# Kernel tuning notes

Hardware: AMD Instinct MI355X
Metric: run time of the kernel (lower is better)

## Reference

```python
import jax, jax.numpy as jnp
import numpy as np

K_KP = 4            # sample_keypoints
RADIUS = 2.0        # sample_radius_m
FEATURE_LEVELS = 2
NUM_HEADS = 8


def _keypoints():
    return jnp.array([[0.0, 0.0, 0.0], [RADIUS, 0.0, 0.0],
                      [0.0, RADIUS, 0.0], [-RADIUS, 0.0, 0.0]], jnp.float32)[:K_KP]


def _bilinear(fmap, grid):
    # fmap [C,H,W], grid [N,2] in [-1,1], align_corners=True, zero padding
    C, H, W = fmap.shape
    x = (grid[:, 0] + 1.0) * 0.5 * (W - 1)
    y = (grid[:, 1] + 1.0) * 0.5 * (H - 1)
    x0 = jnp.floor(x); y0 = jnp.floor(y)
    wx1 = x - x0; wx0 = 1.0 - wx1
    wy1 = y - y0; wy0 = 1.0 - wy1

    def get(xi, yi):
        inb = (xi >= 0) & (xi <= W - 1) & (yi >= 0) & (yi <= H - 1)
        xc = jnp.clip(xi, 0, W - 1).astype(jnp.int32)
        yc = jnp.clip(yi, 0, H - 1).astype(jnp.int32)
        return fmap[:, yc, xc] * inb.astype(fmap.dtype)  # [C,N]

    out = (get(x0, y0) * (wx0 * wy0) + get(x0 + 1, y0) * (wx1 * wy0)
           + get(x0, y0 + 1) * (wx0 * wy1) + get(x0 + 1, y0 + 1) * (wx1 * wy1))
    return out.T  # [N,C]


def _sample_level(fmap, refs, intrinsics, extrinsics):
    # fmap [B,V,C,H,W], refs [B,N,3] with N = Q*K_KP
    B, V, C, H, W = fmap.shape
    N = refs.shape[1]
    ph = jnp.concatenate([refs, jnp.ones((B, N, 1), refs.dtype)], -1)     # [B,N,4]
    cam = jnp.einsum('bvij,bnj->bvni', extrinsics, ph)[..., :3]            # [B,V,N,3]
    uvw = jnp.einsum('bvij,bvnj->bvni', intrinsics, cam)                   # [B,V,N,3]
    z = uvw[..., 2]
    zs = jnp.where(jnp.abs(z) > 1e-6, z, 1e-6)
    gx = 2.0 * (uvw[..., 0] / zs) / (W - 1) - 1.0
    gy = 2.0 * (uvw[..., 1] / zs) / (H - 1) - 1.0
    grid = jnp.stack([gx, gy], -1)                                         # [B,V,N,2]
    samp = jax.vmap(jax.vmap(_bilinear))(fmap, grid)                       # [B,V,N,C]
    valid = (z > 0.0).astype(fmap.dtype)                                   # [B,V,N]
    Q = N // K_KP
    samp = samp.reshape(B, V, Q, K_KP, C)
    valid = valid.reshape(B, V, Q, K_KP)
    s = jnp.einsum('bvqkc,bvqk->bqc', samp, valid)
    cnt = jnp.maximum(valid.sum(axis=(1, 3)), 1.0)[..., None]              # [B,Q,1]
    return s / cnt


def _sampler(features, refs_xyz, intrinsics, extrinsics):
    B, Q = refs_xyz.shape[:2]
    refs = (refs_xyz[:, :, None, :] + _keypoints()[None, None]).reshape(B, Q * K_KP, 3)
    out = jnp.zeros((B, Q, features[0].shape[2]), refs_xyz.dtype)
    for fmap in features[:FEATURE_LEVELS]:
        out = out + _sample_level(fmap, refs, intrinsics, extrinsics)
    return out / float(FEATURE_LEVELS)


def _cross_attn(q_in, ctx, Wq, bq, Wk, bk, Wv, bv, Wo, bo):
    B, Qn, D = q_in.shape
    Kn = ctx.shape[1]
    hd = D // NUM_HEADS
    q = (q_in @ Wq.T + bq).reshape(B, Qn, NUM_HEADS, hd).transpose(0, 2, 1, 3)
    k = (ctx @ Wk.T + bk).reshape(B, Kn, NUM_HEADS, hd).transpose(0, 2, 1, 3)
    v = (ctx @ Wv.T + bv).reshape(B, Kn, NUM_HEADS, hd).transpose(0, 2, 1, 3)
    scores = jnp.einsum('bhqd,bhkd->bhqk', q, k) / jnp.sqrt(jnp.asarray(hd, q.dtype))
    attn = jax.nn.softmax(scores, axis=-1)
    o = jnp.einsum('bhqk,bhkd->bhqd', attn, v).transpose(0, 2, 1, 3).reshape(B, Qn, D)
    return o @ Wo.T + bo


def setup_inputs() -> dict:
    key = jax.random.key(0)
    ks = jax.random.split(key, 10)
    B, V, C, Q = 2, 6, 256, 900
    features0 = jax.random.normal(ks[0], (B, V, C, 64, 176), jnp.float32)
    features1 = jax.random.normal(ks[1], (B, V, C, 32, 88), jnp.float32)
    refs_xyz = jax.random.uniform(ks[2], (B, Q, 3), jnp.float32, -1.0, 1.0) * jnp.array([50.0, 50.0, 1.5])
    K = np.array([[1000.0, 0.0, 800.0], [0.0, 1000.0, 450.0], [0.0, 0.0, 1.0]], np.float32)
    intrinsics = jnp.asarray(np.broadcast_to(K, (B, V, 3, 3)).copy())
    axes = np.array([[0.0, -1.0, 0.0], [0.0, 0.0, -1.0], [1.0, 0.0, 0.0]], np.float32)
    exts = np.zeros((V, 4, 4), np.float32)
    for vi in range(V):
        yaw = 2.0 * np.pi * vi / V
        Rz = np.array([[np.cos(yaw), np.sin(yaw), 0.0], [-np.sin(yaw), np.cos(yaw), 0.0], [0.0, 0.0, 1.0]], np.float32)
        exts[vi, :3, :3] = axes @ Rz
        exts[vi, 3, 3] = 1.0
    extrinsics = jnp.asarray(np.broadcast_to(exts, (B, V, 4, 4)).copy())
    queries = jax.random.normal(ks[3], (B, Q, C), jnp.float32)
    Wq = jax.random.normal(ks[4], (C, C), jnp.float32) * 0.02
    Wk = jax.random.normal(ks[5], (C, C), jnp.float32) * 0.02
    Wv = jax.random.normal(ks[6], (C, C), jnp.float32) * 0.02
    Wo = jax.random.normal(ks[7], (C, C), jnp.float32) * 0.02
    z = jnp.zeros((C,), jnp.float32)
    return {"features0": features0, "features1": features1, "refs_xyz": refs_xyz,
            "intrinsics": intrinsics, "extrinsics": extrinsics, "queries": queries,
            "Wq": Wq, "bq": z, "Wk": Wk, "bk": z, "Wv": Wv, "bv": z, "Wo": Wo, "bo": z}


def reference(features0, features1, refs_xyz, intrinsics, extrinsics, queries,
              Wq, bq, Wk, bk, Wv, bv, Wo, bo):
    sampled = _sampler([features0, features1], refs_xyz, intrinsics, extrinsics)  # [B,Q,C]
    return _cross_attn(queries, sampled, Wq, bq, Wk, bk, Wv, bv, Wo, bo)
```

## Files before the change

### kernel.cpp

```cpp
#include <hip/hip_runtime.h>
#include <math.h>

#define B 2
#define V 6
#define C 256
#define Q 900
#define NH 8
#define HD 32
#define RADIUS 2.0f
#define M_ROWS (B * Q)
#define NT 29
#define SPLITS 4
#define TPS 8
#define RBH (B * NH * Q)

using short8 = __attribute__((ext_vector_type(8))) short;
using f32x4  = __attribute__((ext_vector_type(4))) float;

__device__ __forceinline__ short f2bf(float f) {
    union { float f; unsigned u; } x; x.f = f;
    unsigned r = x.u + 0x7fffu + ((x.u >> 16) & 1u);
    return (short)(r >> 16);
}

__device__ __forceinline__ float kpx(int k) { return (k == 1) ? RADIUS : ((k == 3) ? -RADIUS : 0.f); }
__device__ __forceinline__ float kpy(int k) { return (k == 2) ? RADIUS : 0.f; }

__global__ __launch_bounds__(256)
void sampler_kernel(const float* __restrict__ f0, const float* __restrict__ f1,
                    const float* __restrict__ refs, const float* __restrict__ intr,
                    const float* __restrict__ extr, float* __restrict__ sampled)
{
    int b = blockIdx.x / Q, q = blockIdx.x % Q;
    int t = threadIdx.x;
    __shared__ float sx0[2][24], sy0[2][24], swx1[2][24], swy1[2][24];
    __shared__ float sval[24];

    if (t < 48) {
        int lvl = t / 24, pt = t % 24;
        int v = pt >> 2, kp = pt & 3;
        const float* r = refs + (size_t)(b * Q + q) * 3;
        float px = r[0] + kpx(kp), py = r[1] + kpy(kp), pz = r[2];
        const float* E = extr + (size_t)(b * V + v) * 16;
        float cx = E[0] * px + E[1] * py + E[2]  * pz + E[3];
        float cy = E[4] * px + E[5] * py + E[6]  * pz + E[7];
        float cz = E[8] * px + E[9] * py + E[10] * pz + E[11];
        const float* Km = intr + (size_t)(b * V + v) * 9;
        float u = Km[0] * cx + Km[1] * cy + Km[2] * cz;
        float w = Km[3] * cx + Km[4] * cy + Km[5] * cz;
        float z = Km[6] * cx + Km[7] * cy + Km[8] * cz;
        float zs = (fabsf(z) > 1e-6f) ? z : 1e-6f;
        float ru = u / zs, rv = w / zs;
        const float Wf = lvl ? 87.f : 175.f;
        const float Hf = lvl ? 31.f : 63.f;
        float gx = 2.f * ru / Wf - 1.f;
        float gy = 2.f * rv / Hf - 1.f;
        float x = (gx + 1.f) * 0.5f * Wf;
        float y = (gy + 1.f) * 0.5f * Hf;
        float x0 = floorf(x), y0 = floorf(y);
        sx0[lvl][pt] = x0;  sy0[lvl][pt] = y0;
        swx1[lvl][pt] = x - x0;  swy1[lvl][pt] = y - y0;
        if (lvl == 0) sval[pt] = (z > 0.f) ? 1.f : 0.f;
    }
    __syncthreads();

    float cnt = 0.f;
    #pragma unroll
    for (int i = 0; i < 24; ++i) cnt += sval[i];
    cnt = fmaxf(cnt, 1.f);
    float icnt = 1.f / cnt;

    const int xi = t & 1;
    const int cb = t >> 1;
    const float xif = (float)xi;
    float acc0 = 0.f, acc1 = 0.f;

    #pragma unroll
    for (int lvl = 0; lvl < 2; ++lvl) {
        const int H = lvl ? 32 : 64;
        const int W = lvl ? 88 : 176;
        const int HW = H * W;
        const float* fm = lvl ? f1 : f0;

        float a0 = 0.f, a1 = 0.f;
        for (int i = 0; i < 24; ++i) {
            if (sval[i] == 0.f) continue;
            int v = i >> 2;
            float x0 = sx0[lvl][i], y0 = sy0[lvl][i];
            float wx1v = swx1[lvl][i], wy1v = swy1[lvl][i];
            float xw = xi ? wx1v : (1.f - wx1v);
            float wy0v = 1.f - wy1v;
            float xf = x0 + xif;
            if (!(xf >= 0.f && xf <= (float)(W - 1))) continue;
            int xc = (int)xf;
            const float* bse  = fm + ((size_t)(b * V + v) * C + cb) * (size_t)HW;
            const float* bse2 = bse + (size_t)128 * HW;
            if (y0 >= 0.f && y0 <= (float)(H - 1)) {
                int off = (int)y0 * W + xc;
                float pw = xw * wy0v;
                a0 += bse[off]  * pw;
                a1 += bse2[off] * pw;
            }
            float y1 = y0 + 1.f;
            if (y1 >= 0.f && y1 <= (float)(H - 1)) {
                int off = (int)y1 * W + xc;
                float pw = xw * wy1v;
                a0 += bse[off]  * pw;
                a1 += bse2[off] * pw;
            }
        }
        acc0 += a0 * icnt;
        acc1 += a1 * icnt;
    }
    acc0 *= 0.5f; acc1 *= 0.5f;
    acc0 += __shfl_xor(acc0, 1);
    acc1 += __shfl_xor(acc1, 1);
    float* outp = sampled + (size_t)(b * Q + q) * C;
    if (xi == 0) outp[cb] = acc0;
    else         outp[cb + 128] = acc1;
}

__global__ __launch_bounds__(256)
void wpack4(const float* __restrict__ W0, const float* __restrict__ W1,
            const float* __restrict__ W2, const float* __restrict__ W3,
            short* __restrict__ P0, short* __restrict__ P1,
            short* __restrict__ P2, short* __restrict__ P3)
{
    int gid = blockIdx.x * 256 + threadIdx.x;
    int mat = gid >> 13;
    int rem = gid & 8191;
    int ks = rem >> 10;
    int nt = (rem >> 6) & 15;
    int lane = rem & 63;
    const float* W = (mat == 0) ? W0 : (mat == 1) ? W1 : (mat == 2) ? W2 : W3;
    short* P = (mat == 0) ? P0 : (mat == 1) ? P1 : (mat == 2) ? P2 : P3;
    int n = nt * 16 + (lane & 15);
    int k0 = ks * 32 + 8 * (lane >> 4);
    float4 a = *(const float4*)(W + (size_t)n * C + k0);
    float4 b = *(const float4*)(W + (size_t)n * C + k0 + 4);
    short8 s;
    s[0] = f2bf(a.x); s[1] = f2bf(a.y); s[2] = f2bf(a.z); s[3] = f2bf(a.w);
    s[4] = f2bf(b.x); s[5] = f2bf(b.y); s[6] = f2bf(b.z); s[7] = f2bf(b.w);
    *(short8*)(P + (size_t)((ks * 16 + nt) * 64 + lane) * 8) = s;
}

__device__ __forceinline__ void mgemm_body(const float* __restrict__ A,
                                           const short* __restrict__ Wp,
                                           const float* __restrict__ bias,
                                           float* __restrict__ Y,
                                           int m0, int n0t)
{
    __shared__ __align__(16) short As[64][264];
    const int tid = threadIdx.x;
    const int lane = tid & 63, w = tid >> 6;
    const int l15 = lane & 15, g = lane >> 4;

    {
        int r = tid & 63, part = tid >> 6;
        int gm = m0 + r;
        #pragma unroll
        for (int c = 0; c < 8; ++c) {
            int k = part * 64 + c * 8;
            float4 x = make_float4(0.f, 0.f, 0.f, 0.f);
            float4 y = make_float4(0.f, 0.f, 0.f, 0.f);
            if (gm < M_ROWS) {
                x = *(const float4*)(A + (size_t)gm * C + k);
                y = *(const float4*)(A + (size_t)gm * C + k + 4);
            }
            short8 s;
            s[0] = f2bf(x.x); s[1] = f2bf(x.y); s[2] = f2bf(x.z); s[3] = f2bf(x.w);
            s[4] = f2bf(y.x); s[5] = f2bf(y.y); s[6] = f2bf(y.z); s[7] = f2bf(y.w);
            *(short8*)&As[r][k] = s;
        }
    }
    __syncthreads();

    f32x4 acc[4];
    #pragma unroll
    for (int c = 0; c < 4; ++c) acc[c] = (f32x4){0.f, 0.f, 0.f, 0.f};

    #pragma unroll
    for (int ks = 0; ks < 8; ++ks) {
        short8 af = *(const short8*)&As[16 * w + l15][ks * 32 + 8 * g];
        #pragma unroll
        for (int c = 0; c < 4; ++c) {
            int nt = n0t * 4 + c;
            short8 bf = *(const short8*)(Wp + (size_t)((ks * 16 + nt) * 64 + lane) * 8);
            acc[c] = __builtin_amdgcn_mfma_f32_16x16x32_bf16(af, bf, acc[c], 0, 0, 0);
        }
    }

    #pragma unroll
    for (int c = 0; c < 4; ++c) {
        int n = n0t * 64 + c * 16 + l15;
        float bv = bias[n];
        #pragma unroll
        for (int j = 0; j < 4; ++j) {
            int gm = m0 + 16 * w + 4 * g + j;
            if (gm < M_ROWS) Y[(size_t)gm * C + n] = acc[c][j] + bv;
        }
    }
}

__global__ __launch_bounds__(256)
void gemm_qkv_mfma(const float* __restrict__ Xq, const float* __restrict__ Xs,
                   const short* __restrict__ Pq, const short* __restrict__ Pk,
                   const short* __restrict__ Pv,
                   const float* __restrict__ bq, const float* __restrict__ bk,
                   const float* __restrict__ bv,
                   float* __restrict__ Yq, float* __restrict__ Yk, float* __restrict__ Yv)
{
    int z = blockIdx.z;
    const float* A    = (z == 0) ? Xq : Xs;
    const short* Wp   = (z == 0) ? Pq : (z == 1) ? Pk : Pv;
    const float* bias = (z == 0) ? bq : (z == 1) ? bk : bv;
    float* Y          = (z == 0) ? Yq : (z == 1) ? Yk : Yv;
    mgemm_body(A, Wp, bias, Y, blockIdx.x * 64, blockIdx.y);
}

__global__ __launch_bounds__(256)
void gemm_o_merge(const float* __restrict__ Opart, const float2* __restrict__ ml,
                  const short* __restrict__ Wp, const float* __restrict__ bias,
                  float* __restrict__ Y)
{
    __shared__ __align__(16) short As[64][264];
    const int tid = threadIdx.x;
    const int lane = tid & 63, w = tid >> 6;
    const int l15 = lane & 15, g = lane >> 4;
    const int m0 = blockIdx.x * 64, n0t = blockIdx.y;

    {
        int r = tid & 63, part = tid >> 6;
        int gm = m0 + r;
        if (gm < M_ROWS) {
            int bb = (gm >= Q) ? 1 : 0;
            int qq = gm - bb * Q;
            #pragma unroll
            for (int hh = 0; hh < 2; ++hh) {
                int h = 2 * part + hh;
                int rrow = (bb * NH + h) * Q + qq;
                float2 v[SPLITS];
                float m = -1e30f;
                #pragma unroll
                for (int s = 0; s < SPLITS; ++s) {
                    v[s] = ml[(size_t)s * RBH + rrow];
                    m = fmaxf(m, v[s].x);
                }
                float l = 0.f, wgt[SPLITS];
                #pragma unroll
                for (int s = 0; s < SPLITS; ++s) {
                    wgt[s] = __expf(v[s].x - m);
                    l += v[s].y * wgt[s];
                }
                float invl = 1.f / l;
                #pragma unroll
                for (int cc = 0; cc < 4; ++cc) {
                    int d0 = cc * 8;
                    float o[8] = {0.f,0.f,0.f,0.f,0.f,0.f,0.f,0.f};
                    #pragma unroll
                    for (int s = 0; s < SPLITS; ++s) {
                        const float* op = Opart + ((size_t)s * RBH + rrow) * 32 + d0;
                        float4 x = *(const float4*)op;
                        float4 y = *(const float4*)(op + 4);
                        o[0] += x.x * wgt[s]; o[1] += x.y * wgt[s];
                        o[2] += x.z * wgt[s]; o[3] += x.w * wgt[s];
                        o[4] += y.x * wgt[s]; o[5] += y.y * wgt[s];
                        o[6] += y.z * wgt[s]; o[7] += y.w * wgt[s];
                    }
                    short8 sv;
                    #pragma unroll
                    for (int j = 0; j < 8; ++j) sv[j] = f2bf(o[j] * invl);
                    *(short8*)&As[r][part * 64 + hh * 32 + d0] = sv;
                }
            }
        } else {
            #pragma unroll
            for (int c = 0; c < 8; ++c) {
                short8 z = {0,0,0,0,0,0,0,0};
                *(short8*)&As[r][part * 64 + c * 8] = z;
            }
        }
    }
    __syncthreads();

    f32x4 acc[4];
    #pragma unroll
    for (int c = 0; c < 4; ++c) acc[c] = (f32x4){0.f, 0.f, 0.f, 0.f};

    #pragma unroll
    for (int ks = 0; ks < 8; ++ks) {
        short8 af = *(const short8*)&As[16 * w + l15][ks * 32 + 8 * g];
        #pragma unroll
        for (int c = 0; c < 4; ++c) {
            int nt = n0t * 4 + c;
            short8 bf = *(const short8*)(Wp + (size_t)((ks * 16 + nt) * 64 + lane) * 8);
            acc[c] = __builtin_amdgcn_mfma_f32_16x16x32_bf16(af, bf, acc[c], 0, 0, 0);
        }
    }

    #pragma unroll
    for (int c = 0; c < 4; ++c) {
        int n = n0t * 64 + c * 16 + l15;
        float bv = bias[n];
        #pragma unroll
        for (int j = 0; j < 4; ++j) {
            int gm = m0 + 16 * w + 4 * g + j;
            if (gm < M_ROWS) Y[(size_t)gm * C + n] = acc[c][j] + bv;
        }
    }
}

__global__ __launch_bounds__(128)
void attn_mfma_split(const float* __restrict__ qb, const float* __restrict__ kb,
                     const float* __restrict__ vb,
                     float* __restrict__ Opart, float2* __restrict__ ml)
{
    __shared__ __align__(16) short Ks[2][32][40];
    __shared__ __align__(16) short VT[2][32][36];

    const int tid = threadIdx.x;
    const int lane = tid & 63;
    const int w = tid >> 6;
    const int l15 = lane & 15, g = lane >> 4;
    const int bz = blockIdx.z;
    const int b = bz >> 2, s = bz & 3;
    const int h = blockIdx.y;
    const int q0 = blockIdx.x * 32 + w * 16;
    const int t0 = s * TPS;
    const int t1 = (t0 + TPS < NT) ? (t0 + TPS) : NT;

    short8 qf;
    {
        const float sc = 0.17677669529663687f;
        int qrow = q0 + l15;
        float4 a = make_float4(0.f,0.f,0.f,0.f), c2 = make_float4(0.f,0.f,0.f,0.f);
        if (qrow < Q) {
            const float* p = qb + (size_t)(b * Q + qrow) * C + h * HD + 8 * g;
            a  = *(const float4*)p;
            c2 = *(const float4*)(p + 4);
        }
        qf[0]=f2bf(a.x*sc);  qf[1]=f2bf(a.y*sc);  qf[2]=f2bf(a.z*sc);  qf[3]=f2bf(a.w*sc);
        qf[4]=f2bf(c2.x*sc); qf[5]=f2bf(c2.y*sc); qf[6]=f2bf(c2.z*sc); qf[7]=f2bf(c2.w*sc);
    }

    float m_ = -1e30f, l_ = 0.f;
    f32x4 acc0 = {0.f,0.f,0.f,0.f}, acc1 = {0.f,0.f,0.f,0.f};
    const f32x4 z4 = {0.f,0.f,0.f,0.f};

    const int keyA = tid >> 3,        ccA = tid & 7;
    const int keyB = (128 + tid) >> 3, ccB = tid & 7;
    float4 kregA, vregA, kregB, vregB;

    #define LOAD_TILE(t)                                                        \
    {                                                                           \
        int gkA = (t) * 32 + keyA, gkB = (t) * 32 + keyB;                       \
        if (gkA < Q) {                                                          \
            const float* kp = kb + (size_t)(b*Q+gkA)*C + h*HD + 4*ccA;          \
            const float* vp = vb + (size_t)(b*Q+gkA)*C + h*HD + 4*ccA;          \
            kregA = *(const float4*)kp; vregA = *(const float4*)vp;             \
        } else { kregA = make_float4(0.f,0.f,0.f,0.f); vregA = kregA; }         \
        if (gkB < Q) {                                                          \
            const float* kp = kb + (size_t)(b*Q+gkB)*C + h*HD + 4*ccB;          \
            const float* vp = vb + (size_t)(b*Q+gkB)*C + h*HD + 4*ccB;          \
            kregB = *(const float4*)kp; vregB = *(const float4*)vp;             \
        } else { kregB = make_float4(0.f,0.f,0.f,0.f); vregB = kregB; }         \
    }

    #define WRITE_LDS(bi)                                                       \
    {                                                                           \
        short4 ks;                                                              \
        ks.x = f2bf(kregA.x); ks.y = f2bf(kregA.y); ks.z = f2bf(kregA.z); ks.w = f2bf(kregA.w); \
        *(short4*)&Ks[bi][keyA][4 * ccA] = ks;                                  \
        VT[bi][4*ccA+0][keyA] = f2bf(vregA.x);                                  \
        VT[bi][4*ccA+1][keyA] = f2bf(vregA.y);                                  \
        VT[bi][4*ccA+2][keyA] = f2bf(vregA.z);                                  \
        VT[bi][4*ccA+3][keyA] = f2bf(vregA.w);                                  \
        ks.x = f2bf(kregB.x); ks.y = f2bf(kregB.y); ks.z = f2bf(kregB.z); ks.w = f2bf(kregB.w); \
        *(short4*)&Ks[bi][keyB][4 * ccB] = ks;                                  \
        VT[bi][4*ccB+0][keyB] = f2bf(vregB.x);                                  \
        VT[bi][4*ccB+1][keyB] = f2bf(vregB.y);                                  \
        VT[bi][4*ccB+2][keyB] = f2bf(vregB.z);                                  \
        VT[bi][4*ccB+3][keyB] = f2bf(vregB.w);                                  \
    }

    LOAD_TILE(t0);
    WRITE_LDS(0);
    __syncthreads();

    for (int t = t0; t < t1; ++t) {
        const int buf = (t - t0) & 1;
        if (t + 1 < t1) LOAD_TILE(t + 1);

        short8 kf0 = *(const short8*)&Ks[buf][l15][8 * g];
        short8 kf1 = *(const short8*)&Ks[buf][16 + l15][8 * g];
        f32x4 s0 = __builtin_amdgcn_mfma_f32_16x16x32_bf16(kf0, qf, z4, 0, 0, 0);
        f32x4 s1 = __builtin_amdgcn_mfma_f32_16x16x32_bf16(kf1, qf, z4, 0, 0, 0);

        const int kbase = t * 32;
        if (kbase + 32 > Q) {
            #pragma unroll
            for (int j = 0; j < 4; ++j) {
                if (kbase + 4 * g + j      >= Q) s0[j] = -1e30f;
                if (kbase + 16 + 4 * g + j >= Q) s1[j] = -1e30f;
            }
        }

        float tm = fmaxf(fmaxf(fmaxf(s0[0], s0[1]), fmaxf(s0[2], s0[3])),
                         fmaxf(fmaxf(s1[0], s1[1]), fmaxf(s1[2], s1[3])));
        tm = fmaxf(tm, __shfl_xor(tm, 16));
        tm = fmaxf(tm, __shfl_xor(tm, 32));
        float mn = fmaxf(m_, tm);
        float al = __expf(m_ - mn);
        m_ = mn;
        float p0 = __expf(s0[0]-mn), p1 = __expf(s0[1]-mn), p2 = __expf(s0[2]-mn), p3 = __expf(s0[3]-mn);
        float p4 = __expf(s1[0]-mn), p5 = __expf(s1[1]-mn), p6 = __expf(s1[2]-mn), p7 = __expf(s1[3]-mn);
        float ps = ((p0+p1)+(p2+p3)) + ((p4+p5)+(p6+p7));
        ps += __shfl_xor(ps, 16);
        ps += __shfl_xor(ps, 32);
        l_ = l_ * al + ps;

        #pragma unroll
        for (int j = 0; j < 4; ++j) {
            float alr = __shfl(al, 4 * g + j);
            acc0[j] *= alr;
            acc1[j] *= alr;
        }

        short8 pf;
        pf[0]=f2bf(p0); pf[1]=f2bf(p1); pf[2]=f2bf(p2); pf[3]=f2bf(p3);
        pf[4]=f2bf(p4); pf[5]=f2bf(p5); pf[6]=f2bf(p6); pf[7]=f2bf(p7);

        short4 va  = *(const short4*)&VT[buf][l15][4 * g];
        short4 vb2 = *(const short4*)&VT[buf][l15][16 + 4 * g];
        short4 vc  = *(const short4*)&VT[buf][16 + l15][4 * g];
        short4 vd  = *(const short4*)&VT[buf][16 + l15][16 + 4 * g];
        short8 vf0, vf1;
        vf0[0]=va.x;  vf0[1]=va.y;  vf0[2]=va.z;  vf0[3]=va.w;
        vf0[4]=vb2.x; vf0[5]=vb2.y; vf0[6]=vb2.z; vf0[7]=vb2.w;
        vf1[0]=vc.x;  vf1[1]=vc.y;  vf1[2]=vc.z;  vf1[3]=vc.w;
        vf1[4]=vd.x;  vf1[5]=vd.y;  vf1[6]=vd.z;  vf1[7]=vd.w;
        acc0 = __builtin_amdgcn_mfma_f32_16x16x32_bf16(pf, vf0, acc0, 0, 0, 0);
        acc1 = __builtin_amdgcn_mfma_f32_16x16x32_bf16(pf, vf1, acc1, 0, 0, 0);

        if (t + 1 < t1) WRITE_LDS(buf ^ 1);
        __syncthreads();
    }

    const size_t rowbase = (size_t)((s * B + b) * NH + h) * Q;
    float* op = Opart + rowbase * 32;
    #pragma unroll
    for (int j = 0; j < 4; ++j) {
        int qrow = q0 + 4 * g + j;
        if (qrow < Q) {
            op[(size_t)qrow * 32 + l15]      = acc0[j];
            op[(size_t)qrow * 32 + 16 + l15] = acc1[j];
        }
    }
    if (g == 0 && q0 + l15 < Q) ml[rowbase + q0 + l15] = make_float2(m_, l_);
    #undef LOAD_TILE
    #undef WRITE_LDS
}

extern "C" void kernel_launch(void* const* d_in, const int* in_sizes, int n_in,
                              void* d_out, int out_size, void* d_ws, size_t ws_size,
                              hipStream_t stream) {
    const float* f0   = (const float*)d_in[0];
    const float* f1   = (const float*)d_in[1];
    const float* refs = (const float*)d_in[2];
    const float* intr = (const float*)d_in[3];
    const float* extr = (const float*)d_in[4];
    const float* qin  = (const float*)d_in[5];
    const float* Wq   = (const float*)d_in[6];
    const float* bq   = (const float*)d_in[7];
    const float* Wk   = (const float*)d_in[8];
    const float* bk   = (const float*)d_in[9];
    const float* Wv   = (const float*)d_in[10];
    const float* bv   = (const float*)d_in[11];
    const float* Wo   = (const float*)d_in[12];
    const float* bo   = (const float*)d_in[13];

    float* ws      = (float*)d_ws;
    float* sampled = ws;
    float* qbuf    = sampled + 460800;
    float* kbuf    = qbuf    + 460800;
    float* vbuf    = kbuf    + 460800;
    float* obuf    = vbuf    + 460800;
    short* Pq      = (short*)(obuf + 460800);
    short* Pk      = Pq + 65536;
    short* Pv      = Pk + 65536;
    short* Po      = Pv + 65536;
    float* Opart   = obuf + 460800 + 131072;
    float2* ml     = (float2*)(Opart + (size_t)SPLITS * RBH * 32);
    float* out     = (float*)d_out;

    wpack4<<<128, 256, 0, stream>>>(Wq, Wk, Wv, Wo, Pq, Pk, Pv, Po);

    sampler_kernel<<<B * Q, 256, 0, stream>>>(f0, f1, refs, intr, extr, sampled);

    dim3 ggrid((M_ROWS + 63) / 64, C / 64, 3);
    gemm_qkv_mfma<<<ggrid, 256, 0, stream>>>(qin, sampled, Pq, Pk, Pv,
                                             bq, bk, bv, qbuf, kbuf, vbuf);

    dim3 agrid((Q + 31) / 32, NH, B * SPLITS);
    attn_mfma_split<<<agrid, 128, 0, stream>>>(qbuf, kbuf, vbuf, Opart, ml);

    dim3 ogrid((M_ROWS + 63) / 64, C / 64, 1);
    gemm_o_merge<<<ogrid, 256, 0, stream>>>(Opart, ml, Po, bo, out);
}
```

Measured before the change: 62.79 us.

## Fuse Q projection into sampler launch, drop weight prepack, shrink GEMM tiles

Removes the separate weight-packing kernel; GEMMs now convert fp32 weights to bf16 fragments on the fly. The Q projection runs as extra blocks in the sampler launch, since it does not depend on sampled features. The K/V and output GEMMs use 32-row tiles with 128 threads, giving more blocks. Attention splits go from 4 to 8 to spread work across more CUs. This cuts launch count and fills the GPU better, in exchange for redundant weight conversion per block and more partial results to merge.

```diff
diff --git a/kernel.cpp b/kernel.cpp
--- a/kernel.cpp
+++ b/kernel.cpp
@@ -10,8 +10,8 @@
 #define RADIUS 2.0f
 #define M_ROWS (B * Q)
 #define NT 29
-#define SPLITS 4
-#define TPS 8
+#define SPLITS 8
+#define TPS 4
 #define RBH (B * NH * Q)
 
 using short8 = __attribute__((ext_vector_type(8))) short;
@@ -23,15 +23,91 @@
     return (short)(r >> 16);
 }
 
+__device__ __forceinline__ short8 loadWfrag(const float* __restrict__ W, int n, int k0) {
+    float4 a = *(const float4*)(W + (size_t)n * C + k0);
+    float4 b = *(const float4*)(W + (size_t)n * C + k0 + 4);
+    short8 s;
+    s[0] = f2bf(a.x); s[1] = f2bf(a.y); s[2] = f2bf(a.z); s[3] = f2bf(a.w);
+    s[4] = f2bf(b.x); s[5] = f2bf(b.y); s[6] = f2bf(b.z); s[7] = f2bf(b.w);
+    return s;
+}
+
 __device__ __forceinline__ float kpx(int k) { return (k == 1) ? RADIUS : ((k == 3) ? -RADIUS : 0.f); }
 __device__ __forceinline__ float kpy(int k) { return (k == 2) ? RADIUS : 0.f; }
 
+__device__ void mgemm64_body(const float* __restrict__ A,
+                             const float* __restrict__ W,
+                             const float* __restrict__ bias,
+                             float* __restrict__ Y,
+                             int m0, int n0t)
+{
+    __shared__ __align__(16) short As[64][264];
+    const int tid = threadIdx.x;
+    const int lane = tid & 63, w = tid >> 6;
+    const int l15 = lane & 15, g = lane >> 4;
+
+    {
+        int r = tid & 63, part = tid >> 6;
+        int gm = m0 + r;
+        #pragma unroll
+        for (int c = 0; c < 8; ++c) {
+            int k = part * 64 + c * 8;
+            float4 x = make_float4(0.f, 0.f, 0.f, 0.f);
+            float4 y = make_float4(0.f, 0.f, 0.f, 0.f);
+            if (gm < M_ROWS) {
+                x = *(const float4*)(A + (size_t)gm * C + k);
+                y = *(const float4*)(A + (size_t)gm * C + k + 4);
+            }
+            short8 s;
+            s[0] = f2bf(x.x); s[1] = f2bf(x.y); s[2] = f2bf(x.z); s[3] = f2bf(x.w);
+            s[4] = f2bf(y.x); s[5] = f2bf(y.y); s[6] = f2bf(y.z); s[7] = f2bf(y.w);
+            *(short8*)&As[r][k] = s;
+        }
+    }
+    __syncthreads();
+
+    f32x4 acc[4];
+    #pragma unroll
+    for (int c = 0; c < 4; ++c) acc[c] = (f32x4){0.f, 0.f, 0.f, 0.f};
+
+    #pragma unroll
+    for (int ks = 0; ks < 8; ++ks) {
+        short8 af = *(const short8*)&As[16 * w + l15][ks * 32 + 8 * g];
+        #pragma unroll
+        for (int c = 0; c < 4; ++c) {
+            int nt = n0t * 4 + c;
+            short8 bf = loadWfrag(W, nt * 16 + l15, ks * 32 + 8 * g);
+            acc[c] = __builtin_amdgcn_mfma_f32_16x16x32_bf16(af, bf, acc[c], 0, 0, 0);
+        }
+    }
+
+    #pragma unroll
+    for (int c = 0; c < 4; ++c) {
+        int n = n0t * 64 + c * 16 + l15;
+        float bv = bias[n];
+        #pragma unroll
+        for (int j = 0; j < 4; ++j) {
+            int gm = m0 + 16 * w + 4 * g + j;
+            if (gm < M_ROWS) Y[(size_t)gm * C + n] = acc[c][j] + bv;
+        }
+    }
+}
+
 __global__ __launch_bounds__(256)
-void sampler_kernel(const float* __restrict__ f0, const float* __restrict__ f1,
-                    const float* __restrict__ refs, const float* __restrict__ intr,
-                    const float* __restrict__ extr, float* __restrict__ sampled)
+void sampler_qproj(const float* __restrict__ f0, const float* __restrict__ f1,
+                   const float* __restrict__ refs, const float* __restrict__ intr,
+                   const float* __restrict__ extr, float* __restrict__ sampled,
+                   const float* __restrict__ qin, const float* __restrict__ Wq,
+                   const float* __restrict__ bq, float* __restrict__ qbuf)
 {
-    int b = blockIdx.x / Q, q = blockIdx.x % Q;
+    const int bid = blockIdx.x;
+    if (bid >= B * Q) {
+        int idx = bid - B * Q;
+        mgemm64_body(qin, Wq, bq, qbuf, (idx >> 2) * 64, idx & 3);
+        return;
+    }
+
+    int b = bid / Q, q = bid % Q;
     int t = threadIdx.x;
     __shared__ float sx0[2][24], sy0[2][24], swx1[2][24], swy1[2][24];
     __shared__ float sval[24];
@@ -120,43 +196,25 @@
     else         outp[cb + 128] = acc1;
 }
 
-__global__ __launch_bounds__(256)
-void wpack4(const float* __restrict__ W0, const float* __restrict__ W1,
-            const float* __restrict__ W2, const float* __restrict__ W3,
-            short* __restrict__ P0, short* __restrict__ P1,
-            short* __restrict__ P2, short* __restrict__ P3)
+__global__ __launch_bounds__(128)
+void gemm_kv32(const float* __restrict__ Xs,
+               const float* __restrict__ Wk, const float* __restrict__ Wv,
+               const float* __restrict__ bk, const float* __restrict__ bv,
+               float* __restrict__ Yk, float* __restrict__ Yv)
 {
-    int gid = blockIdx.x * 256 + threadIdx.x;
-    int mat = gid >> 13;
-    int rem = gid & 8191;
-    int ks = rem >> 10;
-    int nt = (rem >> 6) & 15;
-    int lane = rem & 63;
-    const float* W = (mat == 0) ? W0 : (mat == 1) ? W1 : (mat == 2) ? W2 : W3;
-    short* P = (mat == 0) ? P0 : (mat == 1) ? P1 : (mat == 2) ? P2 : P3;
-    int n = nt * 16 + (lane & 15);
-    int k0 = ks * 32 + 8 * (lane >> 4);
-    float4 a = *(const float4*)(W + (size_t)n * C + k0);
-    float4 b = *(const float4*)(W + (size_t)n * C + k0 + 4);
-    short8 s;
-    s[0] = f2bf(a.x); s[1] = f2bf(a.y); s[2] = f2bf(a.z); s[3] = f2bf(a.w);
-    s[4] = f2bf(b.x); s[5] = f2bf(b.y); s[6] = f2bf(b.z); s[7] = f2bf(b.w);
-    *(short8*)(P + (size_t)((ks * 16 + nt) * 64 + lane) * 8) = s;
-}
-
-__device__ __forceinline__ void mgemm_body(const float* __restrict__ A,
-                                           const short* __restrict__ Wp,
-                                           const float* __restrict__ bias,
-                                           float* __restrict__ Y,
-                                           int m0, int n0t)
-{
-    __shared__ __align__(16) short As[64][264];
+    __shared__ __align__(16) short As[32][264];
+    const int z = blockIdx.z;
+    const float* W    = z ? Wv : Wk;
+    const float* bias = z ? bv : bk;
+    float* Y          = z ? Yv : Yk;
+    const int m0 = blockIdx.x * 32, n0t = blockIdx.y;
+
     const int tid = threadIdx.x;
     const int lane = tid & 63, w = tid >> 6;
     const int l15 = lane & 15, g = lane >> 4;
 
     {
-        int r = tid & 63, part = tid >> 6;
+        int r = tid & 31, part = tid >> 5;
         int gm = m0 + r;
         #pragma unroll
         for (int c = 0; c < 8; ++c) {
@@ -164,8 +222,8 @@
             float4 x = make_float4(0.f, 0.f, 0.f, 0.f);
             float4 y = make_float4(0.f, 0.f, 0.f, 0.f);
             if (gm < M_ROWS) {
-                x = *(const float4*)(A + (size_t)gm * C + k);
-                y = *(const float4*)(A + (size_t)gm * C + k + 4);
+                x = *(const float4*)(Xs + (size_t)gm * C + k);
+                y = *(const float4*)(Xs + (size_t)gm * C + k + 4);
             }
             short8 s;
             s[0] = f2bf(x.x); s[1] = f2bf(x.y); s[2] = f2bf(x.z); s[3] = f2bf(x.w);
@@ -185,7 +243,7 @@
         #pragma unroll
         for (int c = 0; c < 4; ++c) {
             int nt = n0t * 4 + c;
-            short8 bf = *(const short8*)(Wp + (size_t)((ks * 16 + nt) * 64 + lane) * 8);
+            short8 bf = loadWfrag(W, nt * 16 + l15, ks * 32 + 8 * g);
             acc[c] = __builtin_amdgcn_mfma_f32_16x16x32_bf16(af, bf, acc[c], 0, 0, 0);
         }
     }
@@ -193,44 +251,28 @@
     #pragma unroll
     for (int c = 0; c < 4; ++c) {
         int n = n0t * 64 + c * 16 + l15;
-        float bv = bias[n];
+        float bv4 = bias[n];
         #pragma unroll
         for (int j = 0; j < 4; ++j) {
             int gm = m0 + 16 * w + 4 * g + j;
-            if (gm < M_ROWS) Y[(size_t)gm * C + n] = acc[c][j] + bv;
-        }
-    }
-}
-
-__global__ __launch_bounds__(256)
-void gemm_qkv_mfma(const float* __restrict__ Xq, const float* __restrict__ Xs,
-                   const short* __restrict__ Pq, const short* __restrict__ Pk,
-                   const short* __restrict__ Pv,
-                   const float* __restrict__ bq, const float* __restrict__ bk,
-                   const float* __restrict__ bv,
-                   float* __restrict__ Yq, float* __restrict__ Yk, float* __restrict__ Yv)
+            if (gm < M_ROWS) Y[(size_t)gm * C + n] = acc[c][j] + bv4;
+        }
+    }
+}
+
+__global__ __launch_bounds__(128)
+void gemm_o_merge32(const float* __restrict__ Opart, const float2* __restrict__ ml,
+                    const float* __restrict__ Wo, const float* __restrict__ bias,
+                    float* __restrict__ Y)
 {
-    int z = blockIdx.z;
-    const float* A    = (z == 0) ? Xq : Xs;
-    const short* Wp   = (z == 0) ? Pq : (z == 1) ? Pk : Pv;
-    const float* bias = (z == 0) ? bq : (z == 1) ? bk : bv;
-    float* Y          = (z == 0) ? Yq : (z == 1) ? Yk : Yv;
-    mgemm_body(A, Wp, bias, Y, blockIdx.x * 64, blockIdx.y);
-}
-
-__global__ __launch_bounds__(256)
-void gemm_o_merge(const float* __restrict__ Opart, const float2* __restrict__ ml,
-                  const short* __restrict__ Wp, const float* __restrict__ bias,
-                  float* __restrict__ Y)
-{
-    __shared__ __align__(16) short As[64][264];
+    __shared__ __align__(16) short As[32][264];
     const int tid = threadIdx.x;
     const int lane = tid & 63, w = tid >> 6;
     const int l15 = lane & 15, g = lane >> 4;
-    const int m0 = blockIdx.x * 64, n0t = blockIdx.y;
+    const int m0 = blockIdx.x * 32, n0t = blockIdx.y;
 
     {
-        int r = tid & 63, part = tid >> 6;
+        int r = tid & 31, part = tid >> 5;
         int gm = m0 + r;
         if (gm < M_ROWS) {
             int bb = (gm >= Q) ? 1 : 0;
@@ -276,31 +318,31 @@
         } else {
             #pragma unroll
             for (int c = 0; c < 8; ++c) {
-                short8 z = {0,0,0,0,0,0,0,0};
-                *(short8*)&As[r][part * 64 + c * 8] = z;
+                short8 zz = {0,0,0,0,0,0,0,0};
+                *(short8*)&As[r][part * 64 + c * 8] = zz;
             }
         }
     }
     __syncthreads();
 
-    f32x4 acc[4];
-    #pragma unroll
-    for (int c = 0; c < 4; ++c) acc[c] = (f32x4){0.f, 0.f, 0.f, 0.f};
+    f32x4 acc[2];
+    acc[0] = (f32x4){0.f, 0.f, 0.f, 0.f};
+    acc[1] = (f32x4){0.f, 0.f, 0.f, 0.f};
 
     #pragma unroll
     for (int ks = 0; ks < 8; ++ks) {
         short8 af = *(const short8*)&As[16 * w + l15][ks * 32 + 8 * g];
         #pragma unroll
-        for (int c = 0; c < 4; ++c) {
-            int nt = n0t * 4 + c;
-            short8 bf = *(const short8*)(Wp + (size_t)((ks * 16 + nt) * 64 + lane) * 8);
+        for (int c = 0; c < 2; ++c) {
+            int nt = n0t * 2 + c;
+            short8 bf = loadWfrag(Wo, nt * 16 + l15, ks * 32 + 8 * g);
             acc[c] = __builtin_amdgcn_mfma_f32_16x16x32_bf16(af, bf, acc[c], 0, 0, 0);
         }
     }
 
     #pragma unroll
-    for (int c = 0; c < 4; ++c) {
-        int n = n0t * 64 + c * 16 + l15;
+    for (int c = 0; c < 2; ++c) {
+        int n = n0t * 32 + c * 16 + l15;
         float bv = bias[n];
         #pragma unroll
         for (int j = 0; j < 4; ++j) {
@@ -323,7 +365,7 @@
     const int w = tid >> 6;
     const int l15 = lane & 15, g = lane >> 4;
     const int bz = blockIdx.z;
-    const int b = bz >> 2, s = bz & 3;
+    const int b = bz >> 3, s = bz & 7;
     const int h = blockIdx.y;
     const int q0 = blockIdx.x * 32 + w * 16;
     const int t0 = s * TPS;
@@ -484,26 +526,19 @@
     float* qbuf    = sampled + 460800;
     float* kbuf    = qbuf    + 460800;
     float* vbuf    = kbuf    + 460800;
-    float* obuf    = vbuf    + 460800;
-    short* Pq      = (short*)(obuf + 460800);
-    short* Pk      = Pq + 65536;
-    short* Pv      = Pk + 65536;
-    short* Po      = Pv + 65536;
-    float* Opart   = obuf + 460800 + 131072;
+    float* Opart   = vbuf + 460800;
     float2* ml     = (float2*)(Opart + (size_t)SPLITS * RBH * 32);
     float* out     = (float*)d_out;
 
-    wpack4<<<128, 256, 0, stream>>>(Wq, Wk, Wv, Wo, Pq, Pk, Pv, Po);
-
-    sampler_kernel<<<B * Q, 256, 0, stream>>>(f0, f1, refs, intr, extr, sampled);
-
-    dim3 ggrid((M_ROWS + 63) / 64, C / 64, 3);
-    gemm_qkv_mfma<<<ggrid, 256, 0, stream>>>(qin, sampled, Pq, Pk, Pv,
-                                             bq, bk, bv, qbuf, kbuf, vbuf);
+    sampler_qproj<<<B * Q + 116, 256, 0, stream>>>(f0, f1, refs, intr, extr,
+                                                   sampled, qin, Wq, bq, qbuf);
+
+    dim3 kvgrid((M_ROWS + 31) / 32, C / 64, 2);
+    gemm_kv32<<<kvgrid, 128, 0, stream>>>(sampled, Wk, Wv, bk, bv, kbuf, vbuf);
 
     dim3 agrid((Q + 31) / 32, NH, B * SPLITS);
     attn_mfma_split<<<agrid, 128, 0, stream>>>(qbuf, kbuf, vbuf, Opart, ml);
 
-    dim3 ogrid((M_ROWS + 63) / 64, C / 64, 1);
-    gemm_o_merge<<<ogrid, 256, 0, stream>>>(Opart, ml, Po, bo, out);
-}
+    dim3 ogrid((M_ROWS + 31) / 32, C / 32, 1);
+    gemm_o_merge32<<<ogrid, 128, 0, stream>>>(Opart, ml, Wo, bo, out);
+}
```

Result: slower. 127.2 us (+102.6%).
